# Kernel tuning notes

Measured on AMD Instinct MI355X. Metric: run time of the kernel, lower is better.

## Reference

```python
import jax, jax.numpy as jnp
import numpy as np

D, N, K, H, F, L, T, V = 2048, 16, 8, 128, 6144, 2, 2048, 32000
EPS = 1e-6
THETA = 1000000.0

def rms_norm(x, scale, eps=EPS):
    x32 = x.astype(jnp.float32)
    y = x32 * jax.lax.rsqrt(jnp.mean(x32 * x32, axis=-1, keepdims=True) + eps)
    return (y * scale).astype(x.dtype)

def apply_rope(x, pos, dim, theta):
    # x: [T, n, H]; rotate_half style RoPE on first `dim` dims (dim == H here)
    half = dim // 2
    inv_freq = 1.0 / (theta ** (jnp.arange(half, dtype=jnp.float32) / half))
    freqs = pos.astype(jnp.float32)[:, None] * inv_freq  # [T, half]
    cos = jnp.cos(freqs)[:, None, :]
    sin = jnp.sin(freqs)[:, None, :]
    x1, x2 = x[..., :half], x[..., half:]
    return jnp.concatenate([x1 * cos - x2 * sin, x2 * cos + x1 * sin], axis=-1).astype(x.dtype)

def qmatmul(x, w, s):
    # fp8 e4m3 dequant matmul: quantize kernel, upcast, scale per output channel
    wq = w.astype(jnp.float8_e4m3fn).astype(jnp.float32)
    return (x @ wq) * s

def setup_inputs() -> dict:
    key = jax.random.key(0)
    ks = jax.random.split(key, 20)
    w = lambda k, sh, sc=0.02: (jax.random.normal(k, sh, jnp.float32) * sc)
    return {
        'input_ids': jax.random.randint(ks[0], (T,), 0, V, jnp.int32),
        'positions': jnp.arange(T, dtype=jnp.int32),
        'embed': w(ks[1], (V, D), 1.0),
        'ln1': jax.random.uniform(ks[2], (L, D), jnp.float32),
        'q_w': w(ks[3], (L, D, N, H)),
        'q_norm': jax.random.uniform(ks[4], (L, H), jnp.float32),
        'k_w': w(ks[5], (L, D, K, H)),
        'k_norm': jax.random.uniform(ks[6], (L, H), jnp.float32),
        'v_w': w(ks[7], (L, D, K, H)),
        'o_w': w(ks[8], (L, N, H, D)),
        'ln2': jax.random.uniform(ks[9], (L, D), jnp.float32),
        'gate_w': w(ks[10], (L, D, F), 0.1),
        'gate_scale': jax.random.uniform(ks[11], (L, F), jnp.float32, 0.01, 0.05),
        'up_w': w(ks[12], (L, D, F), 0.1),
        'up_scale': jax.random.uniform(ks[13], (L, F), jnp.float32, 0.01, 0.05),
        'down_w': w(ks[14], (L, F, D), 0.1),
        'down_scale': jax.random.uniform(ks[15], (L, D), jnp.float32, 0.01, 0.05),
        'final_norm': jax.random.uniform(ks[16], (D,), jnp.float32),
        'lm_head': w(ks[17], (D, V), 0.02),
    }

def reference(input_ids, positions, embed, ln1, q_w, q_norm, k_w, k_norm, v_w, o_w,
              ln2, gate_w, gate_scale, up_w, up_scale, down_w, down_scale,
              final_norm, lm_head):
    h = embed[input_ids]                                   # [T, D]
    t = h.shape[0]
    sm_scale = 1.0 / np.sqrt(H)
    causal = jnp.tril(jnp.ones((t, t), dtype=bool))
    G = N // K  # GQA group size

    def layer(h, p):
        l1, qw, qn, kw, kn, vw, ow, l2, gw, gs, uw, us, dw, ds = p
        x = rms_norm(h, l1)
        q = rms_norm(jnp.einsum('td,dnh->tnh', x, qw), qn)
        q = apply_rope(q, positions, H, THETA)
        k = rms_norm(jnp.einsum('td,dkh->tkh', x, kw), kn)
        k = apply_rope(k, positions, H, THETA)
        v = jnp.einsum('td,dkh->tkh', x, vw)
        qg = q.reshape(t, K, G, H)
        scores = jnp.einsum('tkgh,skh->kgts', qg, k) * sm_scale
        scores = jnp.where(causal[None, None], scores, -1e30)
        attn = jax.nn.softmax(scores, axis=-1)
        o = jnp.einsum('kgts,skh->tkgh', attn, v).reshape(t, N, H)
        h = h + jnp.einsum('tnh,nhd->td', o, ow)
        x2 = rms_norm(h, l2)
        fuse = jax.nn.silu(qmatmul(x2, gw, gs)) * qmatmul(x2, uw, us)
        h = h + qmatmul(fuse, dw, ds)
        return h, None

    h, _ = jax.lax.scan(layer, h, (ln1, q_w, q_norm, k_w, k_norm, v_w, o_w,
                                   ln2, gate_w, gate_scale, up_w, up_scale,
                                   down_w, down_scale))
    h = rms_norm(h, final_norm)
    return h @ lm_head                                      # [T, V] logits
```

## Files before the change

kernel.cpp:

```cpp
#include <hip/hip_runtime.h>

#define TT 2048
#define DD 2048
#define NHEAD 16
#define KHEAD 8
#define HDIM 128
#define FF 6144
#define LLAYERS 2
#define VV 32000

typedef __attribute__((ext_vector_type(8))) __bf16 bf16x8;
typedef __attribute__((ext_vector_type(4))) float f32x4;

__device__ __forceinline__ unsigned short f2bf(float x) {
  unsigned u = __float_as_uint(x);
  return (unsigned short)((u + 0x7FFFu + ((u >> 16) & 1u)) >> 16);
}

__device__ __forceinline__ float fp8_rt(float x) {
  float ax = fabsf(x);
  if (ax < 0.015625f) return rintf(x * 512.0f) * (1.0f / 512.0f);
  unsigned u = __float_as_uint(x);
  unsigned r = (u + 0x7FFFFu + ((u >> 20) & 1u)) & 0xFFF00000u;
  float y = __uint_as_float(r);
  if (fabsf(y) > 448.0f) y = copysignf(448.0f, x);
  return y;
}

__device__ __forceinline__ void gload16(const void* g, void* l) {
  __builtin_amdgcn_global_load_lds((__attribute__((address_space(1))) void*)g,
                                   (__attribute__((address_space(3))) void*)l,
                                   16, 0, 0);
}

__global__ void k_embed_rms(const int* __restrict__ ids, const float* __restrict__ embed,
                            const float* __restrict__ g, float* __restrict__ h,
                            unsigned short* __restrict__ out) {
  int t = blockIdx.x;
  const float4* src = (const float4*)(embed + (size_t)ids[t] * DD);
  float4 a = src[threadIdx.x], b = src[threadIdx.x + 256];
  float4* hrow = (float4*)(h + (size_t)t * DD);
  hrow[threadIdx.x] = a;
  hrow[threadIdx.x + 256] = b;
  float ss = a.x * a.x + a.y * a.y + a.z * a.z + a.w * a.w +
             b.x * b.x + b.y * b.y + b.z * b.z + b.w * b.w;
#pragma unroll
  for (int m = 32; m >= 1; m >>= 1) ss += __shfl_xor(ss, m);
  __shared__ float sred[4];
  int wid = threadIdx.x >> 6;
  if ((threadIdx.x & 63) == 0) sred[wid] = ss;
  __syncthreads();
  float tot = sred[0] + sred[1] + sred[2] + sred[3];
  float rn = 1.0f / sqrtf(tot * (1.0f / 2048.0f) + 1e-6f);
  const float4* gg = (const float4*)g;
  float4 g0 = gg[threadIdx.x], g1 = gg[threadIdx.x + 256];
  unsigned short* o0 = out + (size_t)t * DD + threadIdx.x * 4;
  unsigned short* o1 = o0 + 1024;
  *(ushort4*)o0 = make_ushort4(f2bf(a.x * rn * g0.x), f2bf(a.y * rn * g0.y),
                               f2bf(a.z * rn * g0.z), f2bf(a.w * rn * g0.w));
  *(ushort4*)o1 = make_ushort4(f2bf(b.x * rn * g1.x), f2bf(b.y * rn * g1.y),
                               f2bf(b.z * rn * g1.z), f2bf(b.w * rn * g1.w));
}

__global__ void k_rmsnorm(const float* __restrict__ h, const float* __restrict__ g,
                          unsigned short* __restrict__ out) {
  int t = blockIdx.x;
  const float4* row = (const float4*)(h + (size_t)t * DD);
  float4 a = row[threadIdx.x], b = row[threadIdx.x + 256];
  float ss = a.x * a.x + a.y * a.y + a.z * a.z + a.w * a.w +
             b.x * b.x + b.y * b.y + b.z * b.z + b.w * b.w;
#pragma unroll
  for (int m = 32; m >= 1; m >>= 1) ss += __shfl_xor(ss, m);
  __shared__ float sred[4];
  int wid = threadIdx.x >> 6;
  if ((threadIdx.x & 63) == 0) sred[wid] = ss;
  __syncthreads();
  float tot = sred[0] + sred[1] + sred[2] + sred[3];
  float rn = 1.0f / sqrtf(tot * (1.0f / 2048.0f) + 1e-6f);
  const float4* gg = (const float4*)g;
  float4 g0 = gg[threadIdx.x], g1 = gg[threadIdx.x + 256];
  unsigned short* o0 = out + (size_t)t * DD + threadIdx.x * 4;
  unsigned short* o1 = o0 + 1024;
  *(ushort4*)o0 = make_ushort4(f2bf(a.x * rn * g0.x), f2bf(a.y * rn * g0.y),
                               f2bf(a.z * rn * g0.z), f2bf(a.w * rn * g0.w));
  *(ushort4*)o1 = make_ushort4(f2bf(b.x * rn * g1.x), f2bf(b.y * rn * g1.y),
                               f2bf(b.z * rn * g1.z), f2bf(b.w * rn * g1.w));
}

__global__ void k_sred_rms(const float* __restrict__ dp, const float* __restrict__ ds,
                           float* __restrict__ h, const float* __restrict__ g,
                           unsigned short* __restrict__ out) {
  int t = blockIdx.x;
  float4* hrow = (float4*)(h + (size_t)t * DD);
  float4 a = hrow[threadIdx.x], b = hrow[threadIdx.x + 256];
  float4 pa = {0.f, 0.f, 0.f, 0.f}, pb = {0.f, 0.f, 0.f, 0.f};
#pragma unroll
  for (int s = 0; s < 4; ++s) {
    const float4* pr = (const float4*)(dp + ((size_t)s * TT + t) * DD);
    float4 va = pr[threadIdx.x], vb = pr[threadIdx.x + 256];
    pa.x += va.x; pa.y += va.y; pa.z += va.z; pa.w += va.w;
    pb.x += vb.x; pb.y += vb.y; pb.z += vb.z; pb.w += vb.w;
  }
  if (ds) {
    const float4* dsc = (const float4*)ds;
    float4 s0 = dsc[threadIdx.x], s1 = dsc[threadIdx.x + 256];
    pa.x *= s0.x; pa.y *= s0.y; pa.z *= s0.z; pa.w *= s0.w;
    pb.x *= s1.x; pb.y *= s1.y; pb.z *= s1.z; pb.w *= s1.w;
  }
  a.x += pa.x; a.y += pa.y; a.z += pa.z; a.w += pa.w;
  b.x += pb.x; b.y += pb.y; b.z += pb.z; b.w += pb.w;
  hrow[threadIdx.x] = a;
  hrow[threadIdx.x + 256] = b;
  float ss = a.x * a.x + a.y * a.y + a.z * a.z + a.w * a.w +
             b.x * b.x + b.y * b.y + b.z * b.z + b.w * b.w;
#pragma unroll
  for (int m = 32; m >= 1; m >>= 1) ss += __shfl_xor(ss, m);
  __shared__ float sred[4];
  int wid = threadIdx.x >> 6;
  if ((threadIdx.x & 63) == 0) sred[wid] = ss;
  __syncthreads();
  float tot = sred[0] + sred[1] + sred[2] + sred[3];
  float rn = 1.0f / sqrtf(tot * (1.0f / 2048.0f) + 1e-6f);
  const float4* gg = (const float4*)g;
  float4 g0 = gg[threadIdx.x], g1 = gg[threadIdx.x + 256];
  unsigned short* o0 = out + (size_t)t * DD + threadIdx.x * 4;
  unsigned short* o1 = o0 + 1024;
  *(ushort4*)o0 = make_ushort4(f2bf(a.x * rn * g0.x), f2bf(a.y * rn * g0.y),
                               f2bf(a.z * rn * g0.z), f2bf(a.w * rn * g0.w));
  *(ushort4*)o1 = make_ushort4(f2bf(b.x * rn * g1.x), f2bf(b.y * rn * g1.y),
                               f2bf(b.z * rn * g1.z), f2bf(b.w * rn * g1.w));
}

template <bool QUANT>
__device__ __forceinline__ void wconv_body(const float* W, unsigned short* Wt,
                                           int Kd, int Nd, int bx, int by) {
  __shared__ float tile[64][65];
  int k0 = by * 64, n0 = bx * 64;
  int t = threadIdx.x;
#pragma unroll
  for (int i = 0; i < 4; ++i) {
    int row = (t >> 4) + i * 16, c4 = (t & 15) * 4;
    float4 v = *(const float4*)&W[(size_t)(k0 + row) * Nd + n0 + c4];
    tile[row][c4] = v.x; tile[row][c4 + 1] = v.y;
    tile[row][c4 + 2] = v.z; tile[row][c4 + 3] = v.w;
  }
  __syncthreads();
#pragma unroll
  for (int i = 0; i < 2; ++i) {
    int n = (t >> 3) + i * 32, kc = (t & 7) * 8;
    unsigned short r[8];
#pragma unroll
    for (int j = 0; j < 8; ++j) {
      float x = tile[kc + j][n];
      if (QUANT) x = fp8_rt(x);
      r[j] = f2bf(x);
    }
    unsigned short* o = &Wt[(size_t)(n0 + n) * Kd + k0 + kc];
    *(ushort4*)o = make_ushort4(r[0], r[1], r[2], r[3]);
    *(ushort4*)(o + 4) = make_ushort4(r[4], r[5], r[6], r[7]);
  }
}

template <bool QUANT>
__global__ void k_wconv(const float* __restrict__ W, unsigned short* __restrict__ Wt,
                        int Kd, int Nd) {
  wconv_body<QUANT>(W, Wt, Kd, Nd, blockIdx.x, blockIdx.y);
}

__global__ void k_wconv_qkv(const float* __restrict__ qw, const float* __restrict__ kw,
                            const float* __restrict__ vw, unsigned short* __restrict__ Wt) {
  int b = blockIdx.x;
  if (b < 1024) {
    wconv_body<false>(qw, Wt, DD, 2048, b & 31, b >> 5);
  } else if (b < 1536) {
    int lb = b - 1024;
    wconv_body<false>(kw, Wt + (size_t)2048 * DD, DD, 1024, lb & 15, lb >> 4);
  } else {
    int lb = b - 1536;
    wconv_body<false>(vw, Wt + (size_t)3072 * DD, DD, 1024, lb & 15, lb >> 4);
  }
}

__device__ __forceinline__ void wconv_glu_body(const float* W, unsigned short* Wt,
                                               int bx, int by, int off) {
  __shared__ float tile[64][65];
  int k0 = by * 64, n0 = bx * 64;
  int t = threadIdx.x;
#pragma unroll
  for (int i = 0; i < 4; ++i) {
    int row = (t >> 4) + i * 16, c4 = (t & 15) * 4;
    float4 v = *(const float4*)&W[(size_t)(k0 + row) * FF + n0 + c4];
    tile[row][c4] = v.x; tile[row][c4 + 1] = v.y;
    tile[row][c4 + 2] = v.z; tile[row][c4 + 3] = v.w;
  }
  __syncthreads();
#pragma unroll
  for (int i = 0; i < 2; ++i) {
    int n = (t >> 3) + i * 32, kc = (t & 7) * 8;
    unsigned short r[8];
#pragma unroll
    for (int j = 0; j < 8; ++j) r[j] = f2bf(fp8_rt(tile[kc + j][n]));
    int lj = n0 + n;
    int phys = ((lj >> 4) << 5) + (lj & 15) + off;
    unsigned short* o = &Wt[(size_t)phys * DD + k0 + kc];
    *(ushort4*)o = make_ushort4(r[0], r[1], r[2], r[3]);
    *(ushort4*)(o + 4) = make_ushort4(r[4], r[5], r[6], r[7]);
  }
}

__global__ void k_wconv_glu2(const float* __restrict__ gw, const float* __restrict__ uw,
                             unsigned short* __restrict__ Wt) {
  int b = blockIdx.x;
  if (b < 3072) wconv_glu_body(gw, Wt, b % 96, b / 96, 0);
  else { int lb = b - 3072; wconv_glu_body(uw, Wt, lb % 96, lb / 96, 16); }
}

template <int PT, bool VM, class STG>
__device__ __forceinline__ void gphase(const char* smem, int BUF, int aRd, int bRd,
                                       bf16x8 (&af)[4][2], bf16x8 (&bfr)[2][2][2],
                                       f32x4 (&acc)[8][4], STG&& stage, bool vmzero) {
  constexpr int MH = (PT >= 2) ? 1 : 0;
  constexpr int NH = (PT == 1 || PT == 2) ? 1 : 0;
  if constexpr (PT == 0 || PT == 2) {
#pragma unroll
    for (int m = 0; m < 4; ++m) {
      int abase = BUF + aRd + MH * 8192 + m * 2048;
      af[m][0] = *(const bf16x8*)(smem + abase);
      af[m][1] = *(const bf16x8*)(smem + (abase ^ 64));
    }
  }
  if constexpr (PT <= 1) {
#pragma unroll
    for (int n = 0; n < 2; ++n) {
      int bbase = BUF + bRd + NH * 4096 + n * 2048;
      bfr[NH][n][0] = *(const bf16x8*)(smem + bbase);
      bfr[NH][n][1] = *(const bf16x8*)(smem + (bbase ^ 64));
    }
  }
  stage();
  if (VM) {
    if (vmzero) asm volatile("s_waitcnt vmcnt(0)" ::: "memory");
    else        asm volatile("s_waitcnt vmcnt(4)" ::: "memory");
  }
  __builtin_amdgcn_sched_barrier(0);
  __builtin_amdgcn_s_barrier();
  if constexpr (PT != 3) {
    asm volatile("s_waitcnt lgkmcnt(0)" ::: "memory");
    __builtin_amdgcn_sched_barrier(0);
  }
  __builtin_amdgcn_s_setprio(1);
#pragma unroll
  for (int kk = 0; kk < 2; ++kk)
#pragma unroll
    for (int m = 0; m < 4; ++m)
#pragma unroll
      for (int n = 0; n < 2; ++n)
        acc[MH * 4 + m][NH * 2 + n] = __builtin_amdgcn_mfma_f32_16x16x32_bf16(
            af[m][kk], bfr[NH][n][kk], acc[MH * 4 + m][NH * 2 + n], 0, 0, 0);
  __builtin_amdgcn_s_setprio(0);
  __builtin_amdgcn_sched_barrier(0);
}

template <int EPI>
__global__ __launch_bounds__(512, 2) void k_gemm256(
    const unsigned short* __restrict__ A, const unsigned short* __restrict__ Bt,
    int N, int Kstride, int Kloop, int S, void* __restrict__ Cv,
    const float* __restrict__ gs, const float* __restrict__ us) {
  extern __shared__ __align__(16) char smem[];
  const int tid = threadIdx.x;
  const int lane = tid & 63, wid = tid >> 6;
  const int wm = wid >> 2, wn = wid & 3;
  const int l16 = lane & 15, lg = lane >> 4;
  const int l8 = lane >> 3, s8 = lane & 7;

  const int nwg = gridDim.x;
  const int q = nwg >> 3, r = nwg & 7;
  const int xcd = blockIdx.x & 7, loc = blockIdx.x >> 3;
  const int wg = (xcd < r ? xcd * (q + 1) : r * (q + 1) + (xcd - r) * q) + loc;
  const int bm = wg & 7;
  const int t_ = wg >> 3;
  const int split = t_ % S, bn = t_ / S;
  const size_t m0 = (size_t)bm * 256, n0 = (size_t)bn * 256;
  const size_t kofs = (size_t)split * Kloop;

  const char* Ag = (const char*)(A + m0 * (size_t)Kstride + kofs);
  const char* Bg = (const char*)(Bt + n0 * (size_t)Kstride + kofs);
  const size_t sKA = (size_t)Kstride * 128;
  const size_t sKB = (size_t)Kstride * 64;
  const size_t aA = (size_t)(wid * 8 + l8) * Kstride * 2 + (size_t)((s8 ^ l8) << 4);
  const size_t aB = (size_t)((wid & 3) * 8 + l8) * Kstride * 2 + (size_t)((s8 ^ l8) << 4);

  auto stgA = [&](int BUF, int p, int kt) {
    gload16(Ag + aA + (size_t)p * sKA + (size_t)kt * 128,
            smem + BUF + p * 8192 + wid * 1024);
  };
  auto stgB = [&](int BUF, int qa, int qb, int kt) {
    int qq = (wid < 4) ? qa : qb;
    gload16(Bg + aB + (size_t)qq * sKB + (size_t)kt * 128,
            smem + BUF + 32768 + qq * 4096 + (wid & 3) * 1024);
  };
  auto stAev = [&](int BUF, int kt) { stgA(BUF, 0, kt); stgA(BUF, 2, kt); };
  auto stAod = [&](int BUF, int kt) { stgA(BUF, 1, kt); stgA(BUF, 3, kt); };
  auto stBev = [&](int BUF, int kt) { stgB(BUF, 0, 2, kt); stgB(BUF, 4, 6, kt); };
  auto stBod = [&](int BUF, int kt) { stgB(BUF, 1, 3, kt); stgB(BUF, 5, 7, kt); };

  const int colx = (lg << 4) ^ ((l16 & 7) << 4);
  const int aRd = (wm * 128 + l16) * 128 + colx;
  const int bRd = 32768 + (wn * 64 + l16) * 128 + colx;

  f32x4 acc[8][4] = {};
  bf16x8 af[4][2];
  bf16x8 bfr[2][2][2];

  stAev(0, 0); stAod(0, 0); stBev(0, 0); stBod(0, 0);
  stBev(65536, 1); stBod(65536, 1);
  asm volatile("s_waitcnt vmcnt(4)" ::: "memory");
  __builtin_amdgcn_s_barrier();

  const int NIT = Kloop >> 7;
#pragma unroll 1
  for (int i = 0; i < NIT; ++i) {
    const int t1 = 2 * i + 1, t2 = 2 * i + 2, t3 = 2 * i + 3;
    const bool more = (i + 1 < NIT);
    gphase<0, false>(smem, 0, aRd, bRd, af, bfr, acc, [&] { stAev(65536, t1); }, false);
    gphase<1, false>(smem, 0, aRd, bRd, af, bfr, acc, [&] { stAod(65536, t1); }, false);
    gphase<2, false>(smem, 0, aRd, bRd, af, bfr, acc, [&] { if (more) stBev(0, t2); }, false);
    gphase<3, true >(smem, 0, aRd, bRd, af, bfr, acc, [&] { if (more) stBod(0, t2); }, !more);
    gphase<0, false>(smem, 65536, aRd, bRd, af, bfr, acc, [&] { if (more) stAev(0, t2); }, false);
    gphase<1, false>(smem, 65536, aRd, bRd, af, bfr, acc, [&] { if (more) stAod(0, t2); }, false);
    gphase<2, false>(smem, 65536, aRd, bRd, af, bfr, acc, [&] { if (more) stBev(65536, t3); }, false);
    gphase<3, true >(smem, 65536, aRd, bRd, af, bfr, acc, [&] { if (more) stBod(65536, t3); }, false);
  }

  if constexpr (EPI == 2) {
    const int q0 = (int)((n0 + (size_t)wn * 64) >> 5);
    const float gsc0 = gs[q0 * 16 + l16], usc0 = us[q0 * 16 + l16];
    const float gsc1 = gs[(q0 + 1) * 16 + l16], usc1 = us[(q0 + 1) * 16 + l16];
    unsigned short* F = (unsigned short*)Cv;
#pragma unroll
    for (int m = 0; m < 8; ++m)
#pragma unroll
      for (int rr = 0; rr < 4; ++rr) {
        size_t row = m0 + wm * 128 + m * 16 + lg * 4 + rr;
        float g0 = acc[m][0][rr] * gsc0, u0 = acc[m][1][rr] * usc0;
        float g1 = acc[m][2][rr] * gsc1, u1 = acc[m][3][rr] * usc1;
        F[row * FF + q0 * 16 + l16] = f2bf((g0 / (1.0f + __expf(-g0))) * u0);
        F[row * FF + (q0 + 1) * 16 + l16] = f2bf((g1 / (1.0f + __expf(-g1))) * u1);
      }
  } else {
    char* Cb = (char*)Cv + (EPI == 0 ? (size_t)split * TT * N * 4 : 0);
#pragma unroll
    for (int m = 0; m < 8; ++m)
#pragma unroll
      for (int rr = 0; rr < 4; ++rr) {
        size_t row = m0 + wm * 128 + m * 16 + lg * 4 + rr;
#pragma unroll
        for (int n = 0; n < 4; ++n) {
          size_t col = n0 + wn * 64 + n * 16 + l16;
          float v = acc[m][n][rr];
          size_t idx = row * (size_t)N + col;
          if constexpr (EPI == 0) ((float*)Cb)[idx] = v;
          else ((unsigned short*)Cb)[idx] = f2bf(v);
        }
      }
  }
}

__device__ __forceinline__ void qk_post_body(const float* p0, const float* p1,
                                             const float* nscale, const int* pos,
                                             unsigned short* out, int nheads,
                                             int coloff, float qscale, int bx) {
  int gw = bx * 4 + (threadIdx.x >> 6);
  int t = gw / nheads, n = gw % nheads;
  int lane = threadIdx.x & 63;
  size_t base = (size_t)t * 4096 + coloff + n * HDIM;
  float x1 = p0[base + lane] + p1[base + lane];
  float x2 = p0[base + lane + 64] + p1[base + lane + 64];
  float ss = x1 * x1 + x2 * x2;
#pragma unroll
  for (int m = 32; m >= 1; m >>= 1) ss += __shfl_xor(ss, m);
  float rn = qscale / sqrtf(ss * (1.0f / 128.0f) + 1e-6f);
  x1 *= rn * nscale[lane];
  x2 *= rn * nscale[lane + 64];
  float p = (float)pos[t];
  float inv = powf(1.0e6f, -(float)lane / 64.0f);
  float fr = p * inv;
  float c = cosf(fr), s = sinf(fr);
  unsigned short* o = out + ((size_t)n * TT + t) * HDIM;
  o[lane] = f2bf(x1 * c - x2 * s);
  o[lane + 64] = f2bf(x2 * c + x1 * s);
}

__global__ void k_qkv_post(const float* __restrict__ p0, const float* __restrict__ p1,
                           const float* __restrict__ qn, const float* __restrict__ kn,
                           const int* __restrict__ pos, unsigned short* __restrict__ qb,
                           unsigned short* __restrict__ kb, unsigned short* __restrict__ vT,
                           float qscale) {
  int b = blockIdx.x;
  if (b < 8192) {
    qk_post_body(p0, p1, qn, pos, qb, NHEAD, 0, qscale, b);
  } else if (b < 12288) {
    qk_post_body(p0, p1, kn, pos, kb, KHEAD, 2048, 1.0f, b - 8192);
  } else {
    int lb = b - 12288;
    __shared__ float tile[32][33];
    int t0 = (lb & 63) * 32, h0 = (lb >> 6) * 32;
    int tx = threadIdx.x & 31, ty = threadIdx.x >> 5;
#pragma unroll
    for (int i = 0; i < 32; i += 8) {
      size_t idx = (size_t)(t0 + ty + i) * 4096 + 3072 + h0 + tx;
      tile[ty + i][tx] = p0[idx] + p1[idx];
    }
    __syncthreads();
    int kvh = h0 >> 7;
    int hh = h0 & 127;
#pragma unroll
    for (int i = 0; i < 32; i += 8) {
      float x = tile[tx][ty + i];
      vT[(size_t)kvh * HDIM * TT + (size_t)(hh + ty + i) * TT + t0 + tx] = f2bf(x);
    }
  }
}

__global__ __launch_bounds__(256, 2) void k_attn(
    const unsigned short* __restrict__ Qb, const unsigned short* __restrict__ Kb,
    const unsigned short* __restrict__ Vt, unsigned short* __restrict__ Ob) {
  __shared__ __align__(16) char kv[2][32768];
  __shared__ __align__(16) char Pl[4][2048];
  const int tid = threadIdx.x;
  const int w = tid >> 6, lane = tid & 63;
  const int l16 = lane & 15, lg = lane >> 4;
  const int head = blockIdx.y, kvh = head >> 1;
  const int j = blockIdx.x;
  const int rbase[2] = {j * 64 + w * 16, (31 - j) * 64 + w * 16};

  bf16x8 qf[2][4];
#pragma unroll
  for (int qg = 0; qg < 2; ++qg) {
    const unsigned short* Qrow = Qb + ((size_t)head * TT + rbase[qg] + l16) * HDIM;
#pragma unroll
    for (int kc = 0; kc < 4; ++kc) qf[qg][kc] = *(const bf16x8*)&Qrow[kc * 32 + lg * 8];
  }

  const char* Kh = (const char*)(Kb + (size_t)kvh * TT * HDIM);
  const char* Vh = (const char*)(Vt + (size_t)kvh * HDIM * TT);

  auto stage = [&](int buf, int t) {
    const int kt0 = t * 64;
    char* bk = kv[buf];
    char* bv = kv[buf] + 16384;
#pragma unroll
    for (int it = 0; it < 4; ++it) {
      int rowK = it * 16 + w * 4 + (lane >> 4);
      gload16(Kh + (size_t)(kt0 + rowK) * 256 + (((lane & 15) ^ (rowK & 7)) << 4),
              bk + (it * 256 + w * 64) * 16);
      int rowV = it * 32 + w * 8 + (lane >> 3);
      gload16(Vh + (size_t)rowV * (TT * 2) + (size_t)kt0 * 2 +
                  (((lane & 7) ^ (rowV & 7)) << 4),
              bv + (it * 256 + w * 64) * 16);
    }
  };

  f32x4 o[2][8] = {};
  float m_[2][4], l_[2][4];
#pragma unroll
  for (int qg = 0; qg < 2; ++qg)
#pragma unroll
    for (int r = 0; r < 4; ++r) { m_[qg][r] = -1e30f; l_[qg][r] = 0.0f; }
  char* Pw = Pl[w];

  const int nt = 32 - j;
  stage(0, 0);
  asm volatile("s_waitcnt vmcnt(0)" ::: "memory");
  __syncthreads();

#pragma unroll 1
  for (int t = 0; t < nt; ++t) {
    const int buf = t & 1;
    const int kt0 = t * 64;
    if (t + 1 < nt) stage(buf ^ 1, t + 1);
    const char* bk = kv[buf];
    const char* bv = kv[buf] + 16384;

#pragma unroll
    for (int qg = 0; qg < 2; ++qg) {
      if (qg == 0 && t > j) continue;
      f32x4 sg[4];
#pragma unroll
      for (int cg = 0; cg < 4; ++cg) {
        sg[cg] = f32x4{0.f, 0.f, 0.f, 0.f};
#pragma unroll
        for (int kc = 0; kc < 4; ++kc) {
          int row = cg * 16 + l16;
          int slot = kc * 4 + lg;
          bf16x8 kf = *(const bf16x8*)(bk + row * 256 + ((slot ^ (row & 7)) << 4));
          sg[cg] = __builtin_amdgcn_mfma_f32_16x16x32_bf16(qf[qg][kc], kf, sg[cg], 0, 0, 0);
        }
      }
      f32x4 mx;
#pragma unroll
      for (int r = 0; r < 4; ++r) {
        int row = rbase[qg] + 4 * lg + r;
        float a = sg[0][r]; if (kt0 + l16 > row) a = -1e30f; sg[0][r] = a;
        float b = sg[1][r]; if (kt0 + 16 + l16 > row) b = -1e30f; sg[1][r] = b;
        float c = sg[2][r]; if (kt0 + 32 + l16 > row) c = -1e30f; sg[2][r] = c;
        float d = sg[3][r]; if (kt0 + 48 + l16 > row) d = -1e30f; sg[3][r] = d;
        mx[r] = fmaxf(fmaxf(a, b), fmaxf(c, d));
      }
#pragma unroll
      for (int msk = 8; msk >= 1; msk >>= 1)
#pragma unroll
        for (int r = 0; r < 4; ++r) mx[r] = fmaxf(mx[r], __shfl_xor(mx[r], msk));
      float alpha[4];
#pragma unroll
      for (int r = 0; r < 4; ++r) {
        float mn = fmaxf(m_[qg][r], mx[r]);
        alpha[r] = __expf(m_[qg][r] - mn);
        m_[qg][r] = mn;
      }
      f32x4 rs;
#pragma unroll
      for (int r = 0; r < 4; ++r) {
        float s0 = __expf(sg[0][r] - m_[qg][r]);
        float s1 = __expf(sg[1][r] - m_[qg][r]);
        float s2 = __expf(sg[2][r] - m_[qg][r]);
        float s3 = __expf(sg[3][r] - m_[qg][r]);
        sg[0][r] = s0; sg[1][r] = s1; sg[2][r] = s2; sg[3][r] = s3;
        rs[r] = (s0 + s1) + (s2 + s3);
      }
#pragma unroll
      for (int msk = 8; msk >= 1; msk >>= 1)
#pragma unroll
        for (int r = 0; r < 4; ++r) rs[r] += __shfl_xor(rs[r], msk);
#pragma unroll
      for (int r = 0; r < 4; ++r) l_[qg][r] = l_[qg][r] * alpha[r] + rs[r];
#pragma unroll
      for (int hi = 0; hi < 8; ++hi)
#pragma unroll
        for (int r = 0; r < 4; ++r) o[qg][hi][r] *= alpha[r];

#pragma unroll
      for (int cg = 0; cg < 4; ++cg)
#pragma unroll
        for (int r = 0; r < 4; ++r) {
          int prow = 4 * lg + r;
          int slot = cg * 2 + (l16 >> 3);
          *(unsigned short*)(Pw + prow * 128 + ((slot ^ (prow & 7)) << 4) +
                             (l16 & 7) * 2) = f2bf(sg[cg][r]);
        }
      bf16x8 pf[2];
#pragma unroll
      for (int half = 0; half < 2; ++half) {
        int slot = half * 4 + lg;
        pf[half] = *(const bf16x8*)(Pw + l16 * 128 + ((slot ^ (l16 & 7)) << 4));
      }
#pragma unroll
      for (int hi = 0; hi < 8; ++hi) {
        int row = hi * 16 + l16;
#pragma unroll
        for (int half = 0; half < 2; ++half) {
          int slot = half * 4 + lg;
          bf16x8 vf = *(const bf16x8*)(bv + row * 128 + ((slot ^ (row & 7)) << 4));
          o[qg][hi] = __builtin_amdgcn_mfma_f32_16x16x32_bf16(pf[half], vf, o[qg][hi], 0, 0, 0);
        }
      }
    }
    asm volatile("s_waitcnt vmcnt(0)" ::: "memory");
    __syncthreads();
  }

#pragma unroll
  for (int qg = 0; qg < 2; ++qg)
#pragma unroll
    for (int r = 0; r < 4; ++r) {
      float inv = 1.0f / l_[qg][r];
      size_t t = rbase[qg] + 4 * lg + r;
#pragma unroll
      for (int hi = 0; hi < 8; ++hi)
        Ob[t * DD + head * HDIM + hi * 16 + l16] = f2bf(o[qg][hi][r] * inv);
    }
}

extern "C" void kernel_launch(void* const* d_in, const int* in_sizes, int n_in,
                              void* d_out, int out_size, void* d_ws, size_t ws_size,
                              hipStream_t stream) {
  (void)in_sizes; (void)n_in; (void)out_size; (void)ws_size;
  const int* ids = (const int*)d_in[0];
  const int* pos = (const int*)d_in[1];
  const float* embed = (const float*)d_in[2];
  const float* ln1 = (const float*)d_in[3];
  const float* q_w = (const float*)d_in[4];
  const float* q_norm = (const float*)d_in[5];
  const float* k_w = (const float*)d_in[6];
  const float* k_norm = (const float*)d_in[7];
  const float* v_w = (const float*)d_in[8];
  const float* o_w = (const float*)d_in[9];
  const float* ln2 = (const float*)d_in[10];
  const float* gate_w = (const float*)d_in[11];
  const float* gate_s = (const float*)d_in[12];
  const float* up_w = (const float*)d_in[13];
  const float* up_s = (const float*)d_in[14];
  const float* down_w = (const float*)d_in[15];
  const float* down_s = (const float*)d_in[16];
  const float* fnorm = (const float*)d_in[17];
  const float* lm = (const float*)d_in[18];

  hipFuncSetAttribute((const void*)k_gemm256<0>,
                      hipFuncAttributeMaxDynamicSharedMemorySize, 131072);
  hipFuncSetAttribute((const void*)k_gemm256<1>,
                      hipFuncAttributeMaxDynamicSharedMemorySize, 131072);
  hipFuncSetAttribute((const void*)k_gemm256<2>,
                      hipFuncAttributeMaxDynamicSharedMemorySize, 131072);

  char* p = (char*)d_ws;
  auto alloc = [&](size_t n) { char* r = p; p += (n + 255) & ~(size_t)255; return r; };
  unsigned short* wbuf = (unsigned short*)alloc((size_t)VV * DD * 2);
  float* h = (float*)alloc((size_t)TT * DD * 4);
  unsigned short* xb = (unsigned short*)alloc((size_t)TT * DD * 2);
  float* qkvf = (float*)alloc((size_t)2 * TT * 4096 * 4);
  unsigned short* qb = (unsigned short*)alloc((size_t)NHEAD * TT * HDIM * 2);
  unsigned short* kb = (unsigned short*)alloc((size_t)KHEAD * TT * HDIM * 2);
  unsigned short* vT = (unsigned short*)alloc((size_t)KHEAD * HDIM * TT * 2);
  unsigned short* ob = (unsigned short*)alloc((size_t)TT * DD * 2);
  unsigned short* fuse = (unsigned short*)alloc((size_t)TT * FF * 2);
  float* dpart = (float*)((char*)wbuf + ((size_t)56 << 20));
  float* qpart1 = qkvf + (size_t)TT * 4096;
  const float sm = 0.08838834764831845f;

  k_embed_rms<<<TT, 256, 0, stream>>>(ids, embed, ln1, h, xb);
  for (int l = 0; l < LLAYERS; ++l) {
    k_wconv_qkv<<<2048, 256, 0, stream>>>(
        q_w + (size_t)l * DD * 2048, k_w + (size_t)l * DD * 1024,
        v_w + (size_t)l * DD * 1024, wbuf);
    k_gemm256<0><<<8 * (4096 / 256) * 2, 512, 131072, stream>>>(
        xb, wbuf, 4096, DD, 1024, 2, qkvf, nullptr, nullptr);
    k_qkv_post<<<14336, 256, 0, stream>>>(
        qkvf, qpart1, q_norm + (size_t)l * HDIM, k_norm + (size_t)l * HDIM, pos,
        qb, kb, vT, sm);
    k_attn<<<dim3(16, NHEAD), 256, 0, stream>>>(qb, kb, vT, ob);
    k_wconv<false><<<dim3(DD / 64, 2048 / 64), 256, 0, stream>>>(
        o_w + (size_t)l * 2048 * DD, wbuf, 2048, DD);
    k_gemm256<0><<<8 * (DD / 256) * 4, 512, 131072, stream>>>(
        ob, wbuf, DD, 2048, 512, 4, dpart, nullptr, nullptr);
    k_sred_rms<<<TT, 256, 0, stream>>>(dpart, nullptr, h, ln2 + (size_t)l * DD, xb);
    k_wconv_glu2<<<6144, 256, 0, stream>>>(
        gate_w + (size_t)l * DD * FF, up_w + (size_t)l * DD * FF, wbuf);
    k_gemm256<2><<<8 * (12288 / 256), 512, 131072, stream>>>(
        xb, wbuf, 12288, DD, DD, 1, fuse, gate_s + (size_t)l * FF,
        up_s + (size_t)l * FF);
    k_wconv<true><<<dim3(DD / 64, FF / 64), 256, 0, stream>>>(
        down_w + (size_t)l * FF * DD, wbuf, FF, DD);
    k_gemm256<0><<<8 * (DD / 256) * 4, 512, 131072, stream>>>(
        fuse, wbuf, DD, FF, 1536, 4, dpart, nullptr, nullptr);
    const float* gnext = (l + 1 < LLAYERS) ? (ln1 + (size_t)(l + 1) * DD) : fnorm;
    k_sred_rms<<<TT, 256, 0, stream>>>(dpart, down_s + (size_t)l * DD, h, gnext, xb);
  }
  k_wconv<false><<<dim3(VV / 64, DD / 64), 256, 0, stream>>>(lm, wbuf, DD, VV);
  k_gemm256<0><<<8 * (VV / 256), 512, 131072, stream>>>(
      xb, wbuf, VV, DD, DD, 1, d_out, nullptr, nullptr);
}
```

Baseline: 1.145 ms.

## Split attention KV loop across two blocks and merge partials in a new kernel

Attention now launches twice as many blocks, with each one handling alternating KV tiles (even or odd) and writing unnormalized fp32 partial outputs along with its row max and sum to scratch. A new merge kernel combines the two halves with log-sum-exp weights and writes bf16 output. The aim is better GPU occupancy, since 256 blocks underfill the device. The cost is extra fp32 scratch traffic and one more launch. The unused k_rmsnorm kernel is also removed.

Measured after the change: 1.132 ms. About the same (-1.2%).

```diff
diff --git a/kernel.cpp b/kernel.cpp
--- a/kernel.cpp
+++ b/kernel.cpp
@@ -62,11 +62,30 @@
                                f2bf(b.z * rn * g1.z), f2bf(b.w * rn * g1.w));
 }
 
-__global__ void k_rmsnorm(const float* __restrict__ h, const float* __restrict__ g,
-                          unsigned short* __restrict__ out) {
+__global__ void k_sred_rms(const float* __restrict__ dp, const float* __restrict__ ds,
+                           float* __restrict__ h, const float* __restrict__ g,
+                           unsigned short* __restrict__ out) {
   int t = blockIdx.x;
-  const float4* row = (const float4*)(h + (size_t)t * DD);
-  float4 a = row[threadIdx.x], b = row[threadIdx.x + 256];
+  float4* hrow = (float4*)(h + (size_t)t * DD);
+  float4 a = hrow[threadIdx.x], b = hrow[threadIdx.x + 256];
+  float4 pa = {0.f, 0.f, 0.f, 0.f}, pb = {0.f, 0.f, 0.f, 0.f};
+#pragma unroll
+  for (int s = 0; s < 4; ++s) {
+    const float4* pr = (const float4*)(dp + ((size_t)s * TT + t) * DD);
+    float4 va = pr[threadIdx.x], vb = pr[threadIdx.x + 256];
+    pa.x += va.x; pa.y += va.y; pa.z += va.z; pa.w += va.w;
+    pb.x += vb.x; pb.y += vb.y; pb.z += vb.z; pb.w += vb.w;
+  }
+  if (ds) {
+    const float4* dsc = (const float4*)ds;
+    float4 s0 = dsc[threadIdx.x], s1 = dsc[threadIdx.x + 256];
+    pa.x *= s0.x; pa.y *= s0.y; pa.z *= s0.z; pa.w *= s0.w;
+    pb.x *= s1.x; pb.y *= s1.y; pb.z *= s1.z; pb.w *= s1.w;
+  }
+  a.x += pa.x; a.y += pa.y; a.z += pa.z; a.w += pa.w;
+  b.x += pb.x; b.y += pb.y; b.z += pb.z; b.w += pb.w;
+  hrow[threadIdx.x] = a;
+  hrow[threadIdx.x + 256] = b;
   float ss = a.x * a.x + a.y * a.y + a.z * a.z + a.w * a.w +
              b.x * b.x + b.y * b.y + b.z * b.z + b.w * b.w;
 #pragma unroll
@@ -87,50 +106,6 @@
                                f2bf(b.z * rn * g1.z), f2bf(b.w * rn * g1.w));
 }
 
-__global__ void k_sred_rms(const float* __restrict__ dp, const float* __restrict__ ds,
-                           float* __restrict__ h, const float* __restrict__ g,
-                           unsigned short* __restrict__ out) {
-  int t = blockIdx.x;
-  float4* hrow = (float4*)(h + (size_t)t * DD);
-  float4 a = hrow[threadIdx.x], b = hrow[threadIdx.x + 256];
-  float4 pa = {0.f, 0.f, 0.f, 0.f}, pb = {0.f, 0.f, 0.f, 0.f};
-#pragma unroll
-  for (int s = 0; s < 4; ++s) {
-    const float4* pr = (const float4*)(dp + ((size_t)s * TT + t) * DD);
-    float4 va = pr[threadIdx.x], vb = pr[threadIdx.x + 256];
-    pa.x += va.x; pa.y += va.y; pa.z += va.z; pa.w += va.w;
-    pb.x += vb.x; pb.y += vb.y; pb.z += vb.z; pb.w += vb.w;
-  }
-  if (ds) {
-    const float4* dsc = (const float4*)ds;
-    float4 s0 = dsc[threadIdx.x], s1 = dsc[threadIdx.x + 256];
-    pa.x *= s0.x; pa.y *= s0.y; pa.z *= s0.z; pa.w *= s0.w;
-    pb.x *= s1.x; pb.y *= s1.y; pb.z *= s1.z; pb.w *= s1.w;
-  }
-  a.x += pa.x; a.y += pa.y; a.z += pa.z; a.w += pa.w;
-  b.x += pb.x; b.y += pb.y; b.z += pb.z; b.w += pb.w;
-  hrow[threadIdx.x] = a;
-  hrow[threadIdx.x + 256] = b;
-  float ss = a.x * a.x + a.y * a.y + a.z * a.z + a.w * a.w +
-             b.x * b.x + b.y * b.y + b.z * b.z + b.w * b.w;
-#pragma unroll
-  for (int m = 32; m >= 1; m >>= 1) ss += __shfl_xor(ss, m);
-  __shared__ float sred[4];
-  int wid = threadIdx.x >> 6;
-  if ((threadIdx.x & 63) == 0) sred[wid] = ss;
-  __syncthreads();
-  float tot = sred[0] + sred[1] + sred[2] + sred[3];
-  float rn = 1.0f / sqrtf(tot * (1.0f / 2048.0f) + 1e-6f);
-  const float4* gg = (const float4*)g;
-  float4 g0 = gg[threadIdx.x], g1 = gg[threadIdx.x + 256];
-  unsigned short* o0 = out + (size_t)t * DD + threadIdx.x * 4;
-  unsigned short* o1 = o0 + 1024;
-  *(ushort4*)o0 = make_ushort4(f2bf(a.x * rn * g0.x), f2bf(a.y * rn * g0.y),
-                               f2bf(a.z * rn * g0.z), f2bf(a.w * rn * g0.w));
-  *(ushort4*)o1 = make_ushort4(f2bf(b.x * rn * g1.x), f2bf(b.y * rn * g1.y),
-                               f2bf(b.z * rn * g1.z), f2bf(b.w * rn * g1.w));
-}
-
 template <bool QUANT>
 __device__ __forceinline__ void wconv_body(const float* W, unsigned short* Wt,
                                            int Kd, int Nd, int bx, int by) {
@@ -424,7 +399,8 @@
 
 __global__ __launch_bounds__(256, 2) void k_attn(
     const unsigned short* __restrict__ Qb, const unsigned short* __restrict__ Kb,
-    const unsigned short* __restrict__ Vt, unsigned short* __restrict__ Ob) {
+    const unsigned short* __restrict__ Vt, float* __restrict__ po,
+    float* __restrict__ ml) {
   __shared__ __align__(16) char kv[2][32768];
   __shared__ __align__(16) char Pl[4][2048];
   const int tid = threadIdx.x;
@@ -432,6 +408,7 @@
   const int l16 = lane & 15, lg = lane >> 4;
   const int head = blockIdx.y, kvh = head >> 1;
   const int j = blockIdx.x;
+  const int half = blockIdx.z;
   const int rbase[2] = {j * 64 + w * 16, (31 - j) * 64 + w * 16};
 
   bf16x8 qf[2][4];
@@ -470,15 +447,16 @@
   char* Pw = Pl[w];
 
   const int nt = 32 - j;
-  stage(0, 0);
+  stage(0, half);
   asm volatile("s_waitcnt vmcnt(0)" ::: "memory");
   __syncthreads();
 
+  int itc = 0;
 #pragma unroll 1
-  for (int t = 0; t < nt; ++t) {
-    const int buf = t & 1;
+  for (int t = half; t < nt; t += 2, ++itc) {
+    const int buf = itc & 1;
     const int kt0 = t * 64;
-    if (t + 1 < nt) stage(buf ^ 1, t + 1);
+    if (t + 2 < nt) stage(buf ^ 1, t + 2);
     const char* bk = kv[buf];
     const char* bv = kv[buf] + 16384;
 
@@ -550,18 +528,18 @@
         }
       bf16x8 pf[2];
 #pragma unroll
-      for (int half = 0; half < 2; ++half) {
-        int slot = half * 4 + lg;
-        pf[half] = *(const bf16x8*)(Pw + l16 * 128 + ((slot ^ (l16 & 7)) << 4));
+      for (int hf = 0; hf < 2; ++hf) {
+        int slot = hf * 4 + lg;
+        pf[hf] = *(const bf16x8*)(Pw + l16 * 128 + ((slot ^ (l16 & 7)) << 4));
       }
 #pragma unroll
       for (int hi = 0; hi < 8; ++hi) {
         int row = hi * 16 + l16;
 #pragma unroll
-        for (int half = 0; half < 2; ++half) {
-          int slot = half * 4 + lg;
+        for (int hf = 0; hf < 2; ++hf) {
+          int slot = hf * 4 + lg;
           bf16x8 vf = *(const bf16x8*)(bv + row * 128 + ((slot ^ (row & 7)) << 4));
-          o[qg][hi] = __builtin_amdgcn_mfma_f32_16x16x32_bf16(pf[half], vf, o[qg][hi], 0, 0, 0);
+          o[qg][hi] = __builtin_amdgcn_mfma_f32_16x16x32_bf16(pf[hf], vf, o[qg][hi], 0, 0, 0);
         }
       }
     }
@@ -570,15 +548,51 @@
   }
 
 #pragma unroll
-  for (int qg = 0; qg < 2; ++qg)
+  for (int qg = 0; qg < 2; ++qg) {
+    int sidx = (((j * 16 + head) * 2 + half) << 1) + qg;
+    float* pob = po + (size_t)sidx * 8192;
+    float* mlb = ml + (size_t)sidx * 128;
 #pragma unroll
     for (int r = 0; r < 4; ++r) {
-      float inv = 1.0f / l_[qg][r];
-      size_t t = rbase[qg] + 4 * lg + r;
+      int lrow = w * 16 + 4 * lg + r;
 #pragma unroll
       for (int hi = 0; hi < 8; ++hi)
-        Ob[t * DD + head * HDIM + hi * 16 + l16] = f2bf(o[qg][hi][r] * inv);
-    }
+        pob[lrow * 128 + hi * 16 + l16] = o[qg][hi][r];
+      if (l16 == 0) {
+        mlb[lrow * 2] = m_[qg][r];
+        mlb[lrow * 2 + 1] = l_[qg][r];
+      }
+    }
+  }
+}
+
+__global__ void k_amerge(const float* __restrict__ po, const float* __restrict__ ml,
+                         unsigned short* __restrict__ Ob) {
+  int b = blockIdx.x;
+  int j = b >> 5, head = (b >> 1) & 15, grp = b & 1;
+  int J = j * 16 + head;
+  int s0 = (J << 2) + grp;
+  int s1 = (J << 2) + 2 + grp;
+  const float4* p04 = (const float4*)(po + (size_t)s0 * 8192);
+  const float4* p14 = (const float4*)(po + (size_t)s1 * 8192);
+  const float* ml0 = ml + (size_t)s0 * 128;
+  const float* ml1 = ml + (size_t)s1 * 128;
+  int trowbase = (grp ? (31 - j) : j) * 64;
+  for (int i = threadIdx.x; i < 2048; i += 256) {
+    int row = i >> 5, c4 = i & 31;
+    float m0 = ml0[row * 2], l0 = ml0[row * 2 + 1];
+    float m1 = ml1[row * 2], l1 = ml1[row * 2 + 1];
+    float M = fmaxf(m0, m1);
+    float w0 = __expf(m0 - M), w1 = __expf(m1 - M);
+    float li = 1.0f / (l0 * w0 + l1 * w1);
+    float4 a = p04[i], c = p14[i];
+    unsigned short r0 = f2bf((a.x * w0 + c.x * w1) * li);
+    unsigned short r1 = f2bf((a.y * w0 + c.y * w1) * li);
+    unsigned short r2 = f2bf((a.z * w0 + c.z * w1) * li);
+    unsigned short r3 = f2bf((a.w * w0 + c.w * w1) * li);
+    *(ushort4*)&Ob[(size_t)(trowbase + row) * DD + head * HDIM + c4 * 4] =
+        make_ushort4(r0, r1, r2, r3);
+  }
 }
 
 extern "C" void kernel_launch(void* const* d_in, const int* in_sizes, int n_in,
@@ -625,6 +639,8 @@
   unsigned short* fuse = (unsigned short*)alloc((size_t)TT * FF * 2);
   float* dpart = (float*)((char*)wbuf + ((size_t)56 << 20));
   float* qpart1 = qkvf + (size_t)TT * 4096;
+  float* apo = qkvf;
+  float* aml = qkvf + (size_t)1024 * 8192;
   const float sm = 0.08838834764831845f;
 
   k_embed_rms<<<TT, 256, 0, stream>>>(ids, embed, ln1, h, xb);
@@ -637,7 +653,8 @@
     k_qkv_post<<<14336, 256, 0, stream>>>(
         qkvf, qpart1, q_norm + (size_t)l * HDIM, k_norm + (size_t)l * HDIM, pos,
         qb, kb, vT, sm);
-    k_attn<<<dim3(16, NHEAD), 256, 0, stream>>>(qb, kb, vT, ob);
+    k_attn<<<dim3(16, NHEAD, 2), 256, 0, stream>>>(qb, kb, vT, apo, aml);
+    k_amerge<<<512, 256, 0, stream>>>(apo, aml, ob);
     k_wconv<false><<<dim3(DD / 64, 2048 / 64), 256, 0, stream>>>(
         o_w + (size_t)l * 2048 * DD, wbuf, 2048, DD);
     k_gemm256<0><<<8 * (DD / 256) * 4, 512, 131072, stream>>>(
```
